# Kernel optimization log

Measured on AMD Instinct MI355X. Metric: run time of the kernel, lower is better.

The kernel has to match this reference:

```python
import jax, jax.numpy as jnp
import numpy as np

KS = 7            # kernel_size
DIL = 1           # dilatation
H = 96
W = 96
PAD = DIL * (KS - 1) // 2
SHIFTS = [s * DIL for s in range(KS)]


def stack_kernel(a, axis=-2):
    # a: [B, H+2*PAD, W+2*PAD, C] -> [B, H, W, ks^2, C] (or stacked on `axis`)
    return jnp.stack([a[:, y:H + y, x:W + x] for y in SHIFTS for x in SHIFTS], axis=axis)


def make_padding_mask():
    # zeros inside, -inf in the halo; stacked per window position -> [1,H,W,ks^2]
    z = jnp.pad(jnp.zeros((1, H, W, 1), jnp.float32),
                ((0, 0), (PAD, PAD), (PAD, PAD), (0, 0)),
                constant_values=-jnp.inf)
    return stack_kernel(z, axis=-1)[..., 0, :]  # [1,H,W,ks^2]


def setup_inputs() -> dict:
    key = jax.random.key(0)
    ks = jax.random.split(key, 8)
    B, C, KD, OD = 2, 128, 64, 128
    Q = jax.random.normal(ks[0], (B, H, W, C), jnp.float32)
    K = jax.random.normal(ks[1], (B, H, W, C), jnp.float32)
    V = jax.random.normal(ks[2], (B, H, W, C), jnp.float32)
    s = 1.0 / np.sqrt(C)
    Wq = jax.random.normal(ks[3], (C, KD), jnp.float32) * s
    Wk = jax.random.normal(ks[4], (C, KD), jnp.float32) * s
    Wv = jax.random.normal(ks[5], (C, OD), jnp.float32) * s
    return {"Q": Q, "K": K, "V": V,
            "Wq": Wq, "bq": jnp.zeros((KD,), jnp.float32),
            "Wk": Wk, "bk": jnp.zeros((KD,), jnp.float32),
            "Wv": Wv, "bv": jnp.zeros((OD,), jnp.float32)}


def reference(Q, K, V, Wq, bq, Wk, bk, Wv, bv):
    # Dense projections (key_dim is not None)
    q = Q @ Wq + bq                      # [B,H,W,KD]
    k = K @ Wk + bk                      # [B,H,W,KD]
    Dk = jnp.asarray(q.shape[-1], q.dtype)

    pad4 = ((0, 0), (PAD, PAD), (PAD, PAD), (0, 0))
    k_stk = stack_kernel(jnp.pad(k, pad4), axis=-2)   # [B,H,W,ks^2,KD]
    mask = make_padding_mask()                        # [1,H,W,ks^2]

    # w = Q . K_neighbors + padding mask; softmax over ks^2 window
    w = jnp.einsum('bhwd,bhwkd->bhwk', q, k_stk) + mask
    scores = jax.nn.softmax(w / jnp.sqrt(Dk), axis=-1)  # [B,H,W,ks^2]

    v_stk = stack_kernel(jnp.pad(V, pad4), axis=-2)   # [B,H,W,ks^2,E]
    out = jnp.einsum('bhwk,bhwke->bhwe', scores, v_stk)
    # V_d Dense with relu (out_dim is not None)
    out = jax.nn.relu(out @ Wv + bv)                  # [B,H,W,out_dim]
    return out
```

## Files before the change

### kernel.cpp

```cpp
#include <hip/hip_runtime.h>
#include <math.h>

#define BH 2
#define HH 96
#define WW 96
#define NPIX (BH*HH*WW)

#define TH 8
#define TW 4
#define NH 140

typedef __attribute__((ext_vector_type(8))) short short8;
typedef __attribute__((ext_vector_type(4))) float f32x4;

__device__ __forceinline__ unsigned short f2bf(float f) {
    union { float f; unsigned u; } a; a.f = f;
    return (unsigned short)((a.u + 0x7FFFu + ((a.u >> 16) & 1u)) >> 16);
}
__device__ __forceinline__ unsigned packbf(float lo, float hi) {
    return (unsigned)f2bf(lo) | ((unsigned)f2bf(hi) << 16);
}

#define WT_STRIDE 136

__global__ __launch_bounds__(256) void prep_proj_kernel(
    const float* __restrict__ Qg, const float* __restrict__ Kg,
    const float* __restrict__ Wq, const float* __restrict__ bq,
    const float* __restrict__ Wk, const float* __restrict__ bk,
    const float* __restrict__ Wv,
    unsigned short* __restrict__ q_bf, unsigned short* __restrict__ k_bf,
    unsigned short* __restrict__ WvT)
{
    __shared__ unsigned short WT[64 * WT_STRIDE];
    const int bid = blockIdx.x;
    const int tid = threadIdx.x;

    if (bid < 576) {
        const bool isq = bid < 288;
        const float* __restrict__ X   = isq ? Qg : Kg;
        const float* __restrict__ Wt  = isq ? Wq : Wk;
        const float* __restrict__ bia = isq ? bq : bk;
        unsigned short* __restrict__ Y = isq ? q_bf : k_bf;

        {
            const float4* __restrict__ W4 = reinterpret_cast<const float4*>(Wt);
            #pragma unroll
            for (int i = 0; i < 8; ++i) {
                const int e  = tid + 256 * i;
                const int k  = e >> 4;
                const int n4 = (e & 15) * 4;
                const float4 v = W4[e];
                WT[(n4 + 0) * WT_STRIDE + k] = f2bf(v.x);
                WT[(n4 + 1) * WT_STRIDE + k] = f2bf(v.y);
                WT[(n4 + 2) * WT_STRIDE + k] = f2bf(v.z);
                WT[(n4 + 3) * WT_STRIDE + k] = f2bf(v.w);
            }
        }
        __syncthreads();

        const int lane = tid & 63;
        const int wvv  = tid >> 6;
        const int row0 = ((bid % 288) * 4 + wvv) * 16;
        const int qd = lane >> 4, m = lane & 15;

        short8 afr[4];
        #pragma unroll
        for (int ks = 0; ks < 4; ++ks) {
            const float4* __restrict__ src = reinterpret_cast<const float4*>(
                X + (size_t)(row0 + m) * 128 + ks * 32 + qd * 8);
            const float4 a0 = src[0], a1 = src[1];
            short8 f;
            f[0] = (short)f2bf(a0.x); f[1] = (short)f2bf(a0.y);
            f[2] = (short)f2bf(a0.z); f[3] = (short)f2bf(a0.w);
            f[4] = (short)f2bf(a1.x); f[5] = (short)f2bf(a1.y);
            f[6] = (short)f2bf(a1.z); f[7] = (short)f2bf(a1.w);
            afr[ks] = f;
        }

        #pragma unroll
        for (int n = 0; n < 4; ++n) {
            f32x4 acc = {};
            #pragma unroll
            for (int ks = 0; ks < 4; ++ks) {
                const short8 bfr = *reinterpret_cast<const short8*>(
                    &WT[(n * 16 + m) * WT_STRIDE + ks * 32 + qd * 8]);
                acc = __builtin_amdgcn_mfma_f32_16x16x32_bf16(afr[ks], bfr, acc, 0, 0, 0);
            }
            const int col = n * 16 + m;
            const float bb = bia[col];
            #pragma unroll
            for (int r = 0; r < 4; ++r)
                Y[(size_t)(row0 + qd * 4 + r) * 64 + col] = f2bf(acc[r] + bb);
        }
    } else {
        const int base = (bid - 576) * 1024 + tid * 4;
        #pragma unroll
        for (int i = 0; i < 4; ++i) {
            const int e = base + i;
            WvT[e] = f2bf(Wv[(e & 127) * 128 + (e >> 7)]);
        }
    }
}

#define PS_OFF 0
#define PS_STRIDE 168
#define AS_OFF 5376
#define AS_STRIDE 136
#define SM_OFF 9728
#define V_OFF 10240
#define VS 160
#define LDS_N 30720

__global__ __launch_bounds__(512, 4) void attn_kernel(
    const unsigned short* __restrict__ q_bf, const unsigned short* __restrict__ k_bf,
    const float* __restrict__ V, const unsigned short* __restrict__ WvT,
    const float* __restrict__ bv, float* __restrict__ out)
{
    __shared__ unsigned short lds[LDS_N];
    const int tid  = threadIdx.x;
    const int lane = tid & 63;
    const int wv   = tid >> 6;
    const int mt   = wv & 1;
    const int ng   = wv >> 1;

    const int bid  = blockIdx.x;
    const int bimg = bid / 288;
    const int tidx = bid % 288;
    const int ty = tidx / 24, tx = tidx % 24;
    const int y0 = ty * TH, x0 = tx * TW;

    const int qd = lane >> 4, m = lane & 15;

    float* __restrict__ smf = reinterpret_cast<float*>(&lds[SM_OFF]);

    const int ntbase = (ng < 2) ? ng * 3 : 6 + (ng - 2) * 2;
    const int ntcnt  = (ng < 2) ? 3 : 2;

    short8 qa[2];
    {
        const int py = mt * 4 + (m >> 2), px = m & 3;
        const size_t gq = (size_t)(bimg * HH + y0 + py) * WW + (x0 + px);
        #pragma unroll
        for (int ks = 0; ks < 2; ++ks)
            qa[ks] = *reinterpret_cast<const short8*>(q_bf + gq * 64 + ks * 32 + qd * 8);
    }

    short8 kb[3][2];
    #pragma unroll
    for (int n5 = 0; n5 < 3; ++n5) {
        if (n5 >= ntcnt) break;
        const int h  = (ntbase + n5) * 16 + m;
        const int hy = (h * 6554) >> 16;
        const int hx = h - hy * 10;
        const int iy = y0 - 3 + hy, ix = x0 - 3 + hx;
        const bool ok = ((unsigned)iy < HH) & ((unsigned)ix < WW) & (h < NH);
        const size_t ob = ok ? (size_t)((bimg * HH + iy) * WW + ix) * 64 : 0;
        #pragma unroll
        for (int ks = 0; ks < 2; ++ks)
            kb[n5][ks] = *reinterpret_cast<const short8*>(k_bf + ob + ks * 32 + qd * 8);
    }

    const int q4  = tid & 31;
    const int pp0 = tid >> 5;
    float4 va[5], vb[5];
    #pragma unroll
    for (int rnd = 0; rnd < 5; ++rnd) {
        const int pp  = rnd * 16 + pp0;
        const int p0p = pp * 2;
        int o0, o1;
        {
            const int hy = (p0p * 6554) >> 16;
            const int hx = p0p - hy * 10;
            const int iy = y0 - 3 + hy, ix = x0 - 3 + hx;
            const bool ok = ((unsigned)iy < HH) & ((unsigned)ix < WW) & (p0p < NH);
            o0 = ok ? ((bimg * HH + iy) * WW + ix) : 0;
        }
        {
            const int p1p = p0p + 1;
            const int hy = (p1p * 6554) >> 16;
            const int hx = p1p - hy * 10;
            const int iy = y0 - 3 + hy, ix = x0 - 3 + hx;
            const bool ok = ((unsigned)iy < HH) & ((unsigned)ix < WW) & (p1p < NH);
            o1 = ok ? ((bimg * HH + iy) * WW + ix) : 0;
        }
        va[rnd] = *reinterpret_cast<const float4*>(V + (size_t)o0 * 128 + q4 * 4);
        vb[rnd] = *reinterpret_cast<const float4*>(V + (size_t)o1 * 128 + q4 * 4);
    }

    f32x4 sc[3];
    #pragma unroll
    for (int n5 = 0; n5 < 3; ++n5) {
        if (n5 >= ntcnt) break;
        f32x4 a = {};
        #pragma unroll
        for (int ks = 0; ks < 2; ++ks)
            a = __builtin_amdgcn_mfma_f32_16x16x32_bf16(qa[ks], kb[n5][ks], a, 0, 0, 0);
        sc[n5] = a;
    }

    float sm[4] = {0.f, 0.f, 0.f, 0.f};
    #pragma unroll
    for (int n5 = 0; n5 < 3; ++n5) {
        if (n5 >= ntcnt) break;
        const int h  = (ntbase + n5) * 16 + m;
        const int hy = (h * 6554) >> 16;
        const int hx = h - hy * 10;
        const int iy = y0 - 3 + hy, ix = x0 - 3 + hx;
        const bool imgok = ((unsigned)iy < HH) & ((unsigned)ix < WW) & (h < NH);
        const int py = mt * 4 + qd;
        const int col = (ntbase + n5) * 16 + m;
        #pragma unroll
        for (int r = 0; r < 4; ++r) {
            const bool ok = imgok & ((unsigned)(hy - py) <= 6u) & ((unsigned)(hx - r) <= 6u);
            const float e = ok ? __expf(sc[n5][r] * 0.125f) : 0.f;
            sm[r] += e;
            const int row = mt * 16 + qd * 4 + r;
            lds[PS_OFF + row * PS_STRIDE + col] = f2bf(e);
        }
    }
    #pragma unroll
    for (int r = 0; r < 4; ++r)
        #pragma unroll
        for (int off = 1; off < 16; off <<= 1)
            sm[r] += __shfl_xor(sm[r], off);

    if (m == 0) {
        #pragma unroll
        for (int r = 0; r < 4; ++r) {
            const int row = mt * 16 + qd * 4 + r;
            smf[row * 4 + ng] = sm[r];
        }
    }

    {
        const int fsw = (q4 >> 1) & 7;
        unsigned* __restrict__ vl32 = reinterpret_cast<unsigned*>(&lds[V_OFF]);
        #pragma unroll
        for (int rnd = 0; rnd < 5; ++rnd) {
            const int pp   = rnd * 16 + pp0;
            const int pb   = rnd * 4 + (pp0 >> 2);
            const int sb   = pb ^ ((pb < 16) ? fsw : (fsw & 3));
            const int colw = sb * 4 + (pp & 3);
            const int rb   = q4 * 4;
            vl32[(rb + 0) * (VS / 2) + colw] = packbf(va[rnd].x, vb[rnd].x);
            vl32[(rb + 1) * (VS / 2) + colw] = packbf(va[rnd].y, vb[rnd].y);
            vl32[(rb + 2) * (VS / 2) + colw] = packbf(va[rnd].z, vb[rnd].z);
            vl32[(rb + 3) * (VS / 2) + colw] = packbf(va[rnd].w, vb[rnd].w);
        }
    }
    __syncthreads();

    float fac[4];
    #pragma unroll
    for (int r = 0; r < 4; ++r) {
        const int row = mt * 16 + qd * 4 + r;
        const float S = smf[row * 4 + 0] + smf[row * 4 + 1]
                      + smf[row * 4 + 2] + smf[row * 4 + 3];
        fac[r] = 1.0f / S;
    }

    short8 wf[2][4];
    #pragma unroll
    for (int n2 = 0; n2 < 2; ++n2)
        #pragma unroll
        for (int ks = 0; ks < 4; ++ks)
            wf[n2][ks] = *reinterpret_cast<const short8*>(
                WvT + ((ng * 2 + n2) * 16 + m) * 128 + ks * 32 + qd * 8);

    short8 pa[5];
    #pragma unroll
    for (int ks = 0; ks < 5; ++ks)
        pa[ks] = *reinterpret_cast<const short8*>(
            &lds[PS_OFF + (mt * 16 + m) * PS_STRIDE + ks * 32 + qd * 8]);

    f32x4 oacc[2] = {};
    #pragma unroll
    for (int ks = 0; ks < 5; ++ks) {
        const int kb2 = ks * 4 + qd;
        #pragma unroll
        for (int n2 = 0; n2 < 2; ++n2) {
            const int ch = (ng * 2 + n2) * 16 + m;
            const int f  = (ch >> 3) & 7;
            const int sb = kb2 ^ ((kb2 < 16) ? f : (f & 3));
            const short8 bfr = *reinterpret_cast<const short8*>(
                &lds[V_OFF + ch * VS + sb * 8]);
            oacc[n2] = __builtin_amdgcn_mfma_f32_16x16x32_bf16(pa[ks], bfr, oacc[n2], 0, 0, 0);
        }
    }

    #pragma unroll
    for (int n2 = 0; n2 < 2; ++n2)
        #pragma unroll
        for (int r = 0; r < 4; ++r) {
            const int row = mt * 16 + qd * 4 + r;
            const int col = (ng * 2 + n2) * 16 + m;
            lds[AS_OFF + row * AS_STRIDE + col] = f2bf(oacc[n2][r] * fac[r]);
        }
    __syncthreads();

    short8 aa[4];
    #pragma unroll
    for (int ks = 0; ks < 4; ++ks)
        aa[ks] = *reinterpret_cast<const short8*>(
            &lds[AS_OFF + (mt * 16 + m) * AS_STRIDE + ks * 32 + qd * 8]);

    #pragma unroll
    for (int n2 = 0; n2 < 2; ++n2) {
        const int nt = ng * 2 + n2;
        f32x4 a = {};
        #pragma unroll
        for (int ks = 0; ks < 4; ++ks)
            a = __builtin_amdgcn_mfma_f32_16x16x32_bf16(aa[ks], wf[n2][ks], a, 0, 0, 0);
        const int col = nt * 16 + m;
        const float bb = bv[col];
        #pragma unroll
        for (int r = 0; r < 4; ++r) {
            const int py = mt * 4 + qd, px = r;
            const size_t gp = (size_t)(bimg * HH + y0 + py) * WW + (x0 + px);
            out[gp * 128 + col] = fmaxf(a[r] + bb, 0.f);
        }
    }
}

extern "C" void kernel_launch(void* const* d_in, const int* in_sizes, int n_in,
                              void* d_out, int out_size, void* d_ws, size_t ws_size,
                              hipStream_t stream)
{
    const float* Q  = (const float*)d_in[0];
    const float* K  = (const float*)d_in[1];
    const float* V  = (const float*)d_in[2];
    const float* Wq = (const float*)d_in[3];
    const float* bq = (const float*)d_in[4];
    const float* Wk = (const float*)d_in[5];
    const float* bk = (const float*)d_in[6];
    const float* Wv = (const float*)d_in[7];
    const float* bv = (const float*)d_in[8];
    float* out = (float*)d_out;

    unsigned short* wbase = (unsigned short*)d_ws;
    unsigned short* WvT   = wbase + 16384;
    unsigned short* q_bf  = wbase + 32768;
    unsigned short* k_bf  = q_bf + (size_t)NPIX * 64;

    prep_proj_kernel<<<592, 256, 0, stream>>>(Q, K, Wq, bq, Wk, bk, Wv,
                                              q_bf, k_bf, WvT);
    attn_kernel<<<576, 512, 0, stream>>>(q_bf, k_bf, V, WvT, bv, out);
}
```

Before: 106.1 us.

## Shrink attention LDS footprint, trim halo padding work, raise occupancy

Result: slower. 117.3 us (+10.5%).

```diff
diff --git a/kernel.cpp b/kernel.cpp
--- a/kernel.cpp
+++ b/kernel.cpp
@@ -41,6 +41,20 @@
         const float* __restrict__ Wt  = isq ? Wq : Wk;
         const float* __restrict__ bia = isq ? bq : bk;
         unsigned short* __restrict__ Y = isq ? q_bf : k_bf;
+
+        const int lane = tid & 63;
+        const int wvv  = tid >> 6;
+        const int row0 = ((bid % 288) * 4 + wvv) * 16;
+        const int qd = lane >> 4, m = lane & 15;
+
+        float4 xa[4][2];
+        #pragma unroll
+        for (int ks = 0; ks < 4; ++ks) {
+            const float4* __restrict__ src = reinterpret_cast<const float4*>(
+                X + (size_t)(row0 + m) * 128 + ks * 32 + qd * 8);
+            xa[ks][0] = src[0];
+            xa[ks][1] = src[1];
+        }
 
         {
             const float4* __restrict__ W4 = reinterpret_cast<const float4*>(Wt);
@@ -58,17 +72,10 @@
         }
         __syncthreads();
 
-        const int lane = tid & 63;
-        const int wvv  = tid >> 6;
-        const int row0 = ((bid % 288) * 4 + wvv) * 16;
-        const int qd = lane >> 4, m = lane & 15;
-
         short8 afr[4];
         #pragma unroll
         for (int ks = 0; ks < 4; ++ks) {
-            const float4* __restrict__ src = reinterpret_cast<const float4*>(
-                X + (size_t)(row0 + m) * 128 + ks * 32 + qd * 8);
-            const float4 a0 = src[0], a1 = src[1];
+            const float4 a0 = xa[ks][0], a1 = xa[ks][1];
             short8 f;
             f[0] = (short)f2bf(a0.x); f[1] = (short)f2bf(a0.y);
             f[2] = (short)f2bf(a0.z); f[3] = (short)f2bf(a0.w);
@@ -103,15 +110,15 @@
 }
 
 #define PS_OFF 0
-#define PS_STRIDE 168
-#define AS_OFF 5376
+#define PS_STRIDE 152
+#define SMPAD 144
+#define AS_OFF 0
 #define AS_STRIDE 136
-#define SM_OFF 9728
-#define V_OFF 10240
-#define VS 160
-#define LDS_N 30720
-
-__global__ __launch_bounds__(512, 4) void attn_kernel(
+#define V_OFF 4864
+#define VS 144
+#define LDS_N 23296
+
+__global__ __launch_bounds__(512, 6) void attn_kernel(
     const unsigned short* __restrict__ q_bf, const unsigned short* __restrict__ k_bf,
     const float* __restrict__ V, const unsigned short* __restrict__ WvT,
     const float* __restrict__ bv, float* __restrict__ out)
@@ -131,10 +138,8 @@
 
     const int qd = lane >> 4, m = lane & 15;
 
-    float* __restrict__ smf = reinterpret_cast<float*>(&lds[SM_OFF]);
-
     const int ntbase = (ng < 2) ? ng * 3 : 6 + (ng - 2) * 2;
-    const int ntcnt  = (ng < 2) ? 3 : 2;
+    const int ntcnt  = (ng < 2) ? 3 : ((ng == 2) ? 2 : 1);
 
     short8 qa[2];
     {
@@ -165,6 +170,7 @@
     float4 va[5], vb[5];
     #pragma unroll
     for (int rnd = 0; rnd < 5; ++rnd) {
+        if (rnd == 4 && pp0 >= 8) break;
         const int pp  = rnd * 16 + pp0;
         const int p0p = pp * 2;
         int o0, o1;
@@ -228,7 +234,7 @@
         #pragma unroll
         for (int r = 0; r < 4; ++r) {
             const int row = mt * 16 + qd * 4 + r;
-            smf[row * 4 + ng] = sm[r];
+            *reinterpret_cast<float*>(&lds[PS_OFF + row * PS_STRIDE + SMPAD + ng * 2]) = sm[r];
         }
     }
 
@@ -237,9 +243,10 @@
         unsigned* __restrict__ vl32 = reinterpret_cast<unsigned*>(&lds[V_OFF]);
         #pragma unroll
         for (int rnd = 0; rnd < 5; ++rnd) {
+            if (rnd == 4 && pp0 >= 8) break;
             const int pp   = rnd * 16 + pp0;
             const int pb   = rnd * 4 + (pp0 >> 2);
-            const int sb   = pb ^ ((pb < 16) ? fsw : (fsw & 3));
+            const int sb   = pb ^ ((pb < 16) ? fsw : (fsw & 1));
             const int colw = sb * 4 + (pp & 3);
             const int rb   = q4 * 4;
             vl32[(rb + 0) * (VS / 2) + colw] = packbf(va[rnd].x, vb[rnd].x);
@@ -254,9 +261,9 @@
     #pragma unroll
     for (int r = 0; r < 4; ++r) {
         const int row = mt * 16 + qd * 4 + r;
-        const float S = smf[row * 4 + 0] + smf[row * 4 + 1]
-                      + smf[row * 4 + 2] + smf[row * 4 + 3];
-        fac[r] = 1.0f / S;
+        const float* __restrict__ sp =
+            reinterpret_cast<const float*>(&lds[PS_OFF + row * PS_STRIDE + SMPAD]);
+        fac[r] = 1.0f / (sp[0] + sp[1] + sp[2] + sp[3]);
     }
 
     short8 wf[2][4];
@@ -269,9 +276,17 @@
 
     short8 pa[5];
     #pragma unroll
-    for (int ks = 0; ks < 5; ++ks)
+    for (int ks = 0; ks < 4; ++ks)
         pa[ks] = *reinterpret_cast<const short8*>(
             &lds[PS_OFF + (mt * 16 + m) * PS_STRIDE + ks * 32 + qd * 8]);
+    {
+        short8 z = {};
+        pa[4] = z;
+        if (qd < 2)
+            pa[4] = *reinterpret_cast<const short8*>(
+                &lds[PS_OFF + (mt * 16 + m) * PS_STRIDE + 128 + qd * 8]);
+    }
+    __syncthreads();
 
     f32x4 oacc[2] = {};
     #pragma unroll
@@ -281,7 +296,7 @@
         for (int n2 = 0; n2 < 2; ++n2) {
             const int ch = (ng * 2 + n2) * 16 + m;
             const int f  = (ch >> 3) & 7;
-            const int sb = kb2 ^ ((kb2 < 16) ? f : (f & 3));
+            const int sb = (kb2 < 16) ? (kb2 ^ f) : ((kb2 < 18) ? (kb2 ^ (f & 1)) : 0);
             const short8 bfr = *reinterpret_cast<const short8*>(
                 &lds[V_OFF + ch * VS + sb * 8]);
             oacc[n2] = __builtin_amdgcn_mfma_f32_16x16x32_bf16(pa[ks], bfr, oacc[n2], 0, 0, 0);
```
